# Kernel optimization log

Hardware: AMD Instinct MI355X
Metric: run time of the kernel (lower is better)

Reference implementation:

```python
import jax, jax.numpy as jnp
import numpy as np

WINDOW_SIZE = 11
SIGMA = 1.5
C1 = 0.01 ** 2
C2 = 0.03 ** 2
L1_WEIGHT = 1.0
SSIM_WEIGHT = 1.0


def _gaussian_window(channels, window_size=WINDOW_SIZE, sigma=SIGMA):
    x = np.arange(window_size, dtype=np.float32) - window_size // 2
    g = np.exp(-(x ** 2) / (2.0 * sigma ** 2))
    g = g / g.sum()
    w2d = np.outer(g, g).astype(np.float32)  # [ws, ws]
    # depthwise kernel layout OIHW with I=1, O=channels
    return jnp.asarray(np.tile(w2d[None, None], (channels, 1, 1, 1)))


def _dwconv(x, w):
    pad = WINDOW_SIZE // 2
    return jax.lax.conv_general_dilated(
        x, w, window_strides=(1, 1), padding=[(pad, pad), (pad, pad)],
        dimension_numbers=('NCHW', 'OIHW', 'NCHW'),
        feature_group_count=x.shape[1])


def setup_inputs() -> dict:
    key = jax.random.key(0)
    k1, k2 = jax.random.split(key)
    shape = (16, 3, 512, 512)
    outputs = jax.random.uniform(k1, shape, dtype=jnp.float32)
    labels = jax.random.uniform(k2, shape, dtype=jnp.float32)
    return {"outputs": outputs, "labels": labels}


def reference(outputs, labels):
    img1, img2 = outputs, labels
    channel = img1.shape[1]
    window = _gaussian_window(channel).astype(img1.dtype)

    mu1 = _dwconv(img1, window)
    mu2 = _dwconv(img2, window)
    mu1_sq = mu1 * mu1
    mu2_sq = mu2 * mu2
    mu1_mu2 = mu1 * mu2
    sigma1_sq = _dwconv(img1 * img1, window) - mu1_sq
    sigma2_sq = _dwconv(img2 * img2, window) - mu2_sq
    sigma12 = _dwconv(img1 * img2, window) - mu1_mu2

    ssim_map = ((2 * mu1_mu2 + C1) * (2 * sigma12 + C2)) / (
        (mu1_sq + mu2_sq + C1) * (sigma1_sq + sigma2_sq + C2))
    ssim = jnp.mean(ssim_map)

    l1_loss = jnp.mean(jnp.abs(outputs - labels))
    ssim_loss = 1.0 - ssim
    return L1_WEIGHT * l1_loss + SSIM_WEIGHT * ssim_loss
```

## Files before the change

kernel.cpp:

```cpp
#include <hip/hip_runtime.h>
#include <hip/hip_bf16.h>
#include <math.h>

#define IMG 512
#define TW 64
#define TH 32
#define NTX 8
#define NTY 16
#define NIMG 48
#define NBLOCKS (NTX * NTY * NIMG)
#define NPIX (16LL * 3 * 512 * 512)

#define C1F 0.0001f
#define C2F 0.0009f

#define SROWS 42
#define SR 88

typedef __attribute__((ext_vector_type(4))) short short4v;
typedef __attribute__((ext_vector_type(8))) short short8;
typedef __attribute__((ext_vector_type(4))) float float4v;
typedef __attribute__((ext_vector_type(2))) unsigned uint2v;
typedef __attribute__((ext_vector_type(4))) unsigned uint4v;

__device__ __forceinline__ float4v mfma16(short4v a, short4v b, float4v c) {
#if defined(__HIP_DEVICE_COMPILE__)
    return __builtin_amdgcn_mfma_f32_16x16x16bf16_1k(a, b, c, 0, 0, 0);
#else
    return c;
#endif
}

#define GW0 0.00102838f
#define GW1 0.00759877f
#define GW2 0.03600077f
#define GW3 0.10936069f
#define GW4 0.21300539f
#define GW5 0.26601172f

__device__ __forceinline__ unsigned short f2bf(float f) {
    unsigned u = __builtin_bit_cast(unsigned, f);
    u += 0x7FFF + ((u >> 16) & 1);
    return (unsigned short)(u >> 16);
}
__device__ __forceinline__ unsigned pk2(float a, float b) {
    __hip_bfloat162 h = __float22bfloat162_rn(make_float2(a, b));
    unsigned u;
    __builtin_memcpy(&u, &h, 4);
    return u;
}
__device__ __forceinline__ float bf2f(short s) {
    return __builtin_bit_cast(float, (unsigned)(unsigned short)s << 16);
}

__global__ __launch_bounds__(256, 8)
void ssim_tile_kernel(const float* __restrict__ xg, const float* __restrict__ yg,
                      float* __restrict__ partials) {
    __shared__ unsigned short sbuf[2][SROWS][SR];
    __shared__ unsigned short gwtbl[16];
    __shared__ float red[8];

    const int tid  = threadIdx.x;
    const int lane = tid & 63;
    const int w    = tid >> 6;
    const int q    = lane >> 4;
    const int n16  = lane & 15;

    const int img = blockIdx.z;
    const int r00  = blockIdx.y * TH - 5;
    const int c00a = blockIdx.x * TW - 8;
    const float* __restrict__ xi = xg + (size_t)img * (IMG * IMG);
    const float* __restrict__ yi = yg + (size_t)img * (IMG * IMG);

    if (tid < 16) {
        const float gwf[11] = {GW0, GW1, GW2, GW3, GW4, GW5, GW4, GW3, GW2, GW1, GW0};
        unsigned short v = 0;
        #pragma unroll
        for (int t = 0; t < 11; ++t)
            if (tid == t) v = f2bf(gwf[t]);
        gwtbl[tid] = v;
    }

    float l1_loc = 0.f;
    #pragma unroll
    for (int it = 0; it < 2; ++it) {
        int u = tid + it * 256;
        if (it == 0 || tid < 420 - 256) {
            int pr  = u / 10;
            int g10 = u - pr * 10;
            int pc8 = g10 << 3;
            int gr = r00 + pr, gc = c00a + pc8;
            float4 x0 = make_float4(0.f, 0.f, 0.f, 0.f), x1 = x0;
            float4 y0 = x0, y1 = x0;
            bool rowok = (unsigned)gr < 512u;
            size_t o = (size_t)gr * IMG + gc;
            if (rowok && (unsigned)gc < 512u) {
                x0 = *(const float4*)(xi + o);
                y0 = *(const float4*)(yi + o);
            }
            if (rowok && (unsigned)(gc + 4) < 512u) {
                x1 = *(const float4*)(xi + o + 4);
                y1 = *(const float4*)(yi + o + 4);
            }
            *(uint4v*)&sbuf[0][pr][pc8] = (uint4v){
                pk2(x0.x, x0.y), pk2(x0.z, x0.w), pk2(x1.x, x1.y), pk2(x1.z, x1.w)};
            *(uint4v*)&sbuf[1][pr][pc8] = (uint4v){
                pk2(y0.x, y0.y), pk2(y0.z, y0.w), pk2(y1.x, y1.y), pk2(y1.z, y1.w)};
            if ((unsigned)(pr - 5) <= 31u && (unsigned)(g10 - 1) <= 7u)
                l1_loc += fabsf(x0.x - y0.x) + fabsf(x0.y - y0.y)
                        + fabsf(x0.z - y0.z) + fabsf(x0.w - y0.w)
                        + fabsf(x1.x - y1.x) + fabsf(x1.y - y1.y)
                        + fabsf(x1.z - y1.z) + fabsf(x1.w - y1.w);
        }
    }
    __syncthreads();

    short8 bh;
    short4v bv0, bv1;
    {
        int baseh = q * 8 - n16 - 3;
        #pragma unroll
        for (int j = 0; j < 8; ++j)
            bh[j] = (short)gwtbl[min((unsigned)(baseh + j), 15u)];
        int base0 = q * 4 - n16, base1 = q * 4 + 16 - n16;
        #pragma unroll
        for (int j = 0; j < 4; ++j) {
            bv0[j] = (short)gwtbl[min((unsigned)(base0 + j), 15u)];
            bv1[j] = (short)gwtbl[min((unsigned)(base1 + j), 15u)];
        }
    }

    const float4v zero4 = {0.f, 0.f, 0.f, 0.f};
    uint2v d1[3][4];
    #pragma unroll
    for (int rg = 0; rg < 3; ++rg) {
        int row = rg * 16 + n16;
        if (rg == 2) row = min(row, 41);
        const int co = w * 16 + q * 8;
        short8 ax = *(const short8*)&sbuf[0][row][co];
        short8 ay = *(const short8*)&sbuf[1][row][co];
        uint4v u2, u3;
        #pragma unroll
        for (int jj = 0; jj < 4; ++jj) {
            float xa = bf2f(ax[2 * jj]),     ya = bf2f(ay[2 * jj]);
            float xb = bf2f(ax[2 * jj + 1]), yb = bf2f(ay[2 * jj + 1]);
            u2[jj] = pk2(fmaf(xa, xa, ya * ya), fmaf(xb, xb, yb * yb));
            u3[jj] = pk2(xa * ya, xb * yb);
        }
        float4v d;
        d = __builtin_amdgcn_mfma_f32_16x16x32_bf16(ax, bh, zero4, 0, 0, 0);
        d1[rg][0] = (uint2v){pk2(d[0], d[1]), pk2(d[2], d[3])};
        d = __builtin_amdgcn_mfma_f32_16x16x32_bf16(ay, bh, zero4, 0, 0, 0);
        d1[rg][1] = (uint2v){pk2(d[0], d[1]), pk2(d[2], d[3])};
        d = __builtin_amdgcn_mfma_f32_16x16x32_bf16(
                __builtin_bit_cast(short8, u2), bh, zero4, 0, 0, 0);
        d1[rg][2] = (uint2v){pk2(d[0], d[1]), pk2(d[2], d[3])};
        d = __builtin_amdgcn_mfma_f32_16x16x32_bf16(
                __builtin_bit_cast(short8, u3), bh, zero4, 0, 0, 0);
        d1[rg][3] = (uint2v){pk2(d[0], d[1]), pk2(d[2], d[3])};
    }

    float ssim_loc = 0.f;
    #pragma unroll
    for (int rgp = 0; rgp < 2; ++rgp) {
        float4v acc4[4];
        #pragma unroll
        for (int ch = 0; ch < 4; ++ch) {
            short4v a1 = __builtin_bit_cast(short4v, d1[rgp + 1][ch]);
            short4v a0 = __builtin_bit_cast(short4v, d1[rgp][ch]);
            acc4[ch] = mfma16(a0, bv0, mfma16(a1, bv1, zero4));
        }
        #pragma unroll
        for (int r = 0; r < 4; ++r) {
            float mu1 = acc4[0][r], mu2 = acc4[1][r];
            float e   = acc4[2][r], e12 = acc4[3][r];
            float p = mu1 * mu2;
            float s = fmaf(mu1, mu1, mu2 * mu2);
            float num1 = fmaf(2.f, p, C1F);
            float num2 = fmaf(2.f, e12 - p, C2F);
            float den1 = s + C1F;
            float den2 = (e - s) + C2F;
            ssim_loc = fmaf(num1 * num2, __builtin_amdgcn_rcpf(den1 * den2), ssim_loc);
        }
    }

    #pragma unroll
    for (int off = 32; off > 0; off >>= 1) {
        ssim_loc += __shfl_down(ssim_loc, off);
        l1_loc   += __shfl_down(l1_loc, off);
    }
    if (lane == 0) {
        red[w] = ssim_loc;
        red[4 + w] = l1_loc;
    }
    __syncthreads();
    if (tid == 0) {
        float ss = red[0] + red[1] + red[2] + red[3];
        float ll = red[4] + red[5] + red[6] + red[7];
        int bid = blockIdx.x + NTX * (blockIdx.y + NTY * blockIdx.z);
        partials[bid] = ss;
        partials[NBLOCKS + bid] = ll;
    }
}

__global__ __launch_bounds__(1024)
void finalize_kernel(const float* __restrict__ partials, float* __restrict__ out) {
    __shared__ double rs[16], rl[16];
    const int tid = threadIdx.x;
    double ss = 0.0, ll = 0.0;
    for (int i = tid; i < NBLOCKS; i += 1024) {
        ss += (double)partials[i];
        ll += (double)partials[NBLOCKS + i];
    }
    #pragma unroll
    for (int off = 32; off > 0; off >>= 1) {
        ss += __shfl_down(ss, off);
        ll += __shfl_down(ll, off);
    }
    int wave = tid >> 6, lane = tid & 63;
    if (lane == 0) { rs[wave] = ss; rl[wave] = ll; }
    __syncthreads();
    if (tid == 0) {
        double sst = 0.0, llt = 0.0;
        #pragma unroll
        for (int w = 0; w < 16; ++w) { sst += rs[w]; llt += rl[w]; }
        double invn = 1.0 / (double)NPIX;
        out[0] = (float)(llt * invn + (1.0 - sst * invn));
    }
}

extern "C" void kernel_launch(void* const* d_in, const int* in_sizes, int n_in,
                              void* d_out, int out_size, void* d_ws, size_t ws_size,
                              hipStream_t stream) {
    const float* x = (const float*)d_in[0];
    const float* y = (const float*)d_in[1];
    float* out = (float*)d_out;
    float* partials = (float*)d_ws;

    dim3 grid(NTX, NTY, NIMG);
    ssim_tile_kernel<<<grid, dim3(256), 0, stream>>>(x, y, partials);
    finalize_kernel<<<1, dim3(1024), 0, stream>>>(partials, out);
}
```

Measured before the change: 136.7 us.

## Load tiles straight from global into MFMA operands, bypassing LDS staging

Drops the shared-memory staging buffer. Each lane now reads its 8 columns for x and y straight from global memory into registers, packs them to bf16, and feeds the horizontal MFMA pass, with the L1 sum folded into the same loop. This removes the LDS write and read traffic and the bf16 decode step, and the products x², y² and xy are now formed in fp32 before rounding. In exchange, overlapping columns between waves are fetched twice from global or L2, access is scattered by row across lanes, and the occupancy hint in the launch bounds is lowered from 8 to 6.

```diff
diff --git a/kernel.cpp b/kernel.cpp
--- a/kernel.cpp
+++ b/kernel.cpp
@@ -14,8 +14,6 @@
 #define C1F 0.0001f
 #define C2F 0.0009f
 
-#define SROWS 42
-#define SR 88
 
 typedef __attribute__((ext_vector_type(4))) short short4v;
 typedef __attribute__((ext_vector_type(8))) short short8;
@@ -49,14 +47,10 @@
     __builtin_memcpy(&u, &h, 4);
     return u;
 }
-__device__ __forceinline__ float bf2f(short s) {
-    return __builtin_bit_cast(float, (unsigned)(unsigned short)s << 16);
-}
-
-__global__ __launch_bounds__(256, 8)
+
+__global__ __launch_bounds__(256, 6)
 void ssim_tile_kernel(const float* __restrict__ xg, const float* __restrict__ yg,
                       float* __restrict__ partials) {
-    __shared__ unsigned short sbuf[2][SROWS][SR];
     __shared__ unsigned short gwtbl[16];
     __shared__ float red[8];
 
@@ -80,39 +74,6 @@
             if (tid == t) v = f2bf(gwf[t]);
         gwtbl[tid] = v;
     }
-
-    float l1_loc = 0.f;
-    #pragma unroll
-    for (int it = 0; it < 2; ++it) {
-        int u = tid + it * 256;
-        if (it == 0 || tid < 420 - 256) {
-            int pr  = u / 10;
-            int g10 = u - pr * 10;
-            int pc8 = g10 << 3;
-            int gr = r00 + pr, gc = c00a + pc8;
-            float4 x0 = make_float4(0.f, 0.f, 0.f, 0.f), x1 = x0;
-            float4 y0 = x0, y1 = x0;
-            bool rowok = (unsigned)gr < 512u;
-            size_t o = (size_t)gr * IMG + gc;
-            if (rowok && (unsigned)gc < 512u) {
-                x0 = *(const float4*)(xi + o);
-                y0 = *(const float4*)(yi + o);
-            }
-            if (rowok && (unsigned)(gc + 4) < 512u) {
-                x1 = *(const float4*)(xi + o + 4);
-                y1 = *(const float4*)(yi + o + 4);
-            }
-            *(uint4v*)&sbuf[0][pr][pc8] = (uint4v){
-                pk2(x0.x, x0.y), pk2(x0.z, x0.w), pk2(x1.x, x1.y), pk2(x1.z, x1.w)};
-            *(uint4v*)&sbuf[1][pr][pc8] = (uint4v){
-                pk2(y0.x, y0.y), pk2(y0.z, y0.w), pk2(y1.x, y1.y), pk2(y1.z, y1.w)};
-            if ((unsigned)(pr - 5) <= 31u && (unsigned)(g10 - 1) <= 7u)
-                l1_loc += fabsf(x0.x - y0.x) + fabsf(x0.y - y0.y)
-                        + fabsf(x0.z - y0.z) + fabsf(x0.w - y0.w)
-                        + fabsf(x1.x - y1.x) + fabsf(x1.y - y1.y)
-                        + fabsf(x1.z - y1.z) + fabsf(x1.w - y1.w);
-        }
-    }
     __syncthreads();
 
     short8 bh;
@@ -130,27 +91,46 @@
         }
     }
 
+    const int cbase = c00a + w * 16 + q * 8;
+    const bool colok = (unsigned)cbase < 512u;
     const float4v zero4 = {0.f, 0.f, 0.f, 0.f};
+    const float4 zf = make_float4(0.f, 0.f, 0.f, 0.f);
+
     uint2v d1[3][4];
+    float l1_loc = 0.f;
     #pragma unroll
     for (int rg = 0; rg < 3; ++rg) {
-        int row = rg * 16 + n16;
-        if (rg == 2) row = min(row, 41);
-        const int co = w * 16 + q * 8;
-        short8 ax = *(const short8*)&sbuf[0][row][co];
-        short8 ay = *(const short8*)&sbuf[1][row][co];
-        uint4v u2, u3;
-        #pragma unroll
-        for (int jj = 0; jj < 4; ++jj) {
-            float xa = bf2f(ax[2 * jj]),     ya = bf2f(ay[2 * jj]);
-            float xb = bf2f(ax[2 * jj + 1]), yb = bf2f(ay[2 * jj + 1]);
-            u2[jj] = pk2(fmaf(xa, xa, ya * ya), fmaf(xb, xb, yb * yb));
-            u3[jj] = pk2(xa * ya, xb * yb);
-        }
+        const int srow = rg * 16 + n16;
+        const int row  = (rg == 2) ? min(srow, 41) : srow;
+        const int gr   = r00 + row;
+        const bool ok  = colok && (unsigned)gr < 512u;
+        float4 xf0 = zf, xf1 = zf, yf0 = zf, yf1 = zf;
+        if (ok) {
+            const size_t o = (size_t)gr * IMG + cbase;
+            xf0 = *(const float4*)(xi + o);
+            xf1 = *(const float4*)(xi + o + 4);
+            yf0 = *(const float4*)(yi + o);
+            yf1 = *(const float4*)(yi + o + 4);
+        }
+        uint4v ux = (uint4v){pk2(xf0.x, xf0.y), pk2(xf0.z, xf0.w),
+                             pk2(xf1.x, xf1.y), pk2(xf1.z, xf1.w)};
+        uint4v uy = (uint4v){pk2(yf0.x, yf0.y), pk2(yf0.z, yf0.w),
+                             pk2(yf1.x, yf1.y), pk2(yf1.z, yf1.w)};
+        uint4v u2 = (uint4v){
+            pk2(fmaf(xf0.x, xf0.x, yf0.x * yf0.x), fmaf(xf0.y, xf0.y, yf0.y * yf0.y)),
+            pk2(fmaf(xf0.z, xf0.z, yf0.z * yf0.z), fmaf(xf0.w, xf0.w, yf0.w * yf0.w)),
+            pk2(fmaf(xf1.x, xf1.x, yf1.x * yf1.x), fmaf(xf1.y, xf1.y, yf1.y * yf1.y)),
+            pk2(fmaf(xf1.z, xf1.z, yf1.z * yf1.z), fmaf(xf1.w, xf1.w, yf1.w * yf1.w))};
+        uint4v u3 = (uint4v){
+            pk2(xf0.x * yf0.x, xf0.y * yf0.y), pk2(xf0.z * yf0.z, xf0.w * yf0.w),
+            pk2(xf1.x * yf1.x, xf1.y * yf1.y), pk2(xf1.z * yf1.z, xf1.w * yf1.w)};
+
         float4v d;
-        d = __builtin_amdgcn_mfma_f32_16x16x32_bf16(ax, bh, zero4, 0, 0, 0);
+        d = __builtin_amdgcn_mfma_f32_16x16x32_bf16(
+                __builtin_bit_cast(short8, ux), bh, zero4, 0, 0, 0);
         d1[rg][0] = (uint2v){pk2(d[0], d[1]), pk2(d[2], d[3])};
-        d = __builtin_amdgcn_mfma_f32_16x16x32_bf16(ay, bh, zero4, 0, 0, 0);
+        d = __builtin_amdgcn_mfma_f32_16x16x32_bf16(
+                __builtin_bit_cast(short8, uy), bh, zero4, 0, 0, 0);
         d1[rg][1] = (uint2v){pk2(d[0], d[1]), pk2(d[2], d[3])};
         d = __builtin_amdgcn_mfma_f32_16x16x32_bf16(
                 __builtin_bit_cast(short8, u2), bh, zero4, 0, 0, 0);
@@ -158,6 +138,12 @@
         d = __builtin_amdgcn_mfma_f32_16x16x32_bf16(
                 __builtin_bit_cast(short8, u3), bh, zero4, 0, 0, 0);
         d1[rg][3] = (uint2v){pk2(d[0], d[1]), pk2(d[2], d[3])};
+
+        if ((unsigned)(q - 1) <= 1u && (unsigned)(srow - 5) <= 31u)
+            l1_loc += fabsf(xf0.x - yf0.x) + fabsf(xf0.y - yf0.y)
+                    + fabsf(xf0.z - yf0.z) + fabsf(xf0.w - yf0.w)
+                    + fabsf(xf1.x - yf1.x) + fabsf(xf1.y - yf1.y)
+                    + fabsf(xf1.z - yf1.z) + fabsf(xf1.w - yf1.w);
     }
 
     float ssim_loc = 0.f;
```

Result: slower. 162.8 us (+19.1%).
